# Kernel optimization log

Measured on AMD Instinct MI355X. Metric: run time of the kernel, lower is better.

Reference implementation:

```python
import jax, jax.numpy as jnp
import numpy as np

N_NODES = 50000


def gcn_layer(x, src, dst, W, b):
    # GCNConv: out = D^{-1/2} (A + I) D^{-1/2} (x W) + b
    n = x.shape[0]
    h = x @ W  # [N, C_out]
    # degree including self-loop (count of incoming edges at dst + 1)
    deg = jnp.zeros((n,), dtype=x.dtype).at[dst].add(1.0) + 1.0
    dinv_sqrt = jax.lax.rsqrt(deg)
    norm = dinv_sqrt[src] * dinv_sqrt[dst]  # [E]
    agg = jax.ops.segment_sum(h[src] * norm[:, None], dst, num_segments=n)
    # self-loop contribution: norm_ii = 1/deg_i
    agg = agg + h * (dinv_sqrt * dinv_sqrt)[:, None]
    return agg + b


def setup_inputs() -> dict:
    key = jax.random.key(0)
    k1, k2, k3, k4, k5, k6 = jax.random.split(key, 6)
    in_c, hid_c, out_c = 128, 128, 64
    x = jax.random.normal(k1, (N_NODES, in_c), dtype=jnp.float32)
    edge_index = jax.random.randint(k2, (2, 600000), 0, N_NODES, dtype=jnp.int64)
    W1 = jax.random.normal(k3, (in_c, hid_c), dtype=jnp.float32) * (1.0 / np.sqrt(in_c))
    b1 = jnp.zeros((hid_c,), dtype=jnp.float32)
    W2 = jax.random.normal(k4, (hid_c, out_c), dtype=jnp.float32) * (1.0 / np.sqrt(hid_c))
    b2 = jnp.zeros((out_c,), dtype=jnp.float32)
    return {"x": x, "edge_index": edge_index, "W1": W1, "b1": b1, "W2": W2, "b2": b2}


def reference(x, edge_index, W1, b1, W2, b2):
    src, dst = edge_index[0], edge_index[1]
    h = gcn_layer(x, src, dst, W1, b1)
    h = jax.nn.relu(h)
    out = gcn_layer(h, src, dst, W2, b2)
    return out
```

## Files before the change

kernel.cpp:

```cpp
#include <hip/hip_runtime.h>

#define IN_C 128
#define HID_C 128
#define OUT_C 64
#define CAP 40
#define LSTR 40

typedef unsigned int uint;
typedef unsigned short ushort;
typedef __attribute__((ext_vector_type(8))) short short8;
typedef __attribute__((ext_vector_type(4))) float f32x4;

__device__ __forceinline__ float bf2f(ushort u) {
    return __uint_as_float(((uint)u) << 16);
}
__device__ __forceinline__ float bfl(uint u) {
    return __uint_as_float(u << 16);
}
__device__ __forceinline__ float bfh(uint u) {
    return __uint_as_float(u & 0xffff0000u);
}
__device__ __forceinline__ ushort f2bf(float f) {
    uint u = __float_as_uint(f);
    return (ushort)((u + 0x7fffu + ((u >> 16) & 1u)) >> 16);
}


__global__ void prep0_kernel(int* __restrict__ cursor, int n,
                             const float* __restrict__ W1, ushort* __restrict__ w1h,
                             ushort* __restrict__ w1l, const float* __restrict__ W2,
                             ushort* __restrict__ w2h, ushort* __restrict__ w2l) {
    int idx = blockIdx.x * blockDim.x + threadIdx.x;
    if (idx < n) {
        cursor[idx] = 0;
    } else if (idx < n + 128 * 128) {
        int i1 = idx - n;
        int k = i1 >> 7, c = i1 & 127;
        float w = W1[i1];
        ushort h = f2bf(w);
        ushort l = f2bf(w - bf2f(h));
        w1h[c * 128 + k] = h;
        w1l[c * 128 + k] = l;
    } else if (idx < n + 128 * 128 + 128 * 64) {
        int i2 = idx - n - 128 * 128;
        int k = i2 >> 6, c = i2 & 63;
        float w = W2[i2];
        ushort h = f2bf(w);
        ushort l = f2bf(w - bf2f(h));
        w2h[c * 128 + k] = h;
        w2l[c * 128 + k] = l;
    }
}


__global__ __launch_bounds__(256) void gemm1_edge_kernel(
    const float* __restrict__ A, const ushort* __restrict__ BTh,
    const ushort* __restrict__ BTl, ushort* __restrict__ C, int M, int gblocks,
    const int* __restrict__ src, const int* __restrict__ dst,
    int* __restrict__ cursor, int* __restrict__ csr_src, int E) {
    constexpr int BN = 128;
    constexpr int NT = BN / 16;
    __shared__ ushort sAh[64 * LSTR], sAl[64 * LSTR];
    __shared__ ushort sBh[BN * LSTR], sBl[BN * LSTR];

    const int tid = threadIdx.x;

    if (blockIdx.x >= gblocks) {
        int e = (blockIdx.x - gblocks) * 256 + tid;
        if (e < E) {
            unsigned s = (unsigned)src[e];
            unsigned d = (unsigned)dst[e];
            if (s < (unsigned)M && d < (unsigned)M) {
                int p = atomicAdd(&cursor[d], 1);
                if (p < CAP) csr_src[d * CAP + p] = (int)s;
            }
        }
        return;
    }

    const int w = tid >> 6;
    const int lane = tid & 63;
    const int m = lane & 15;
    const int quad = lane >> 4;
    const int r0 = blockIdx.x * 64;

    f32x4 acc[NT];
#pragma unroll
    for (int t = 0; t < NT; ++t) acc[t] = (f32x4){0.f, 0.f, 0.f, 0.f};

    for (int k0 = 0; k0 < 128; k0 += 32) {
#pragma unroll
        for (int it = 0; it < 2; ++it) {
            int idx = tid + it * 256;
            int row = idx >> 3;
            int c4 = idx & 7;
            int grow = r0 + row;
            float4 v = make_float4(0.f, 0.f, 0.f, 0.f);
            if (grow < M) v = *(const float4*)&A[(size_t)grow * 128 + k0 + c4 * 4];
            ushort h0 = f2bf(v.x), h1 = f2bf(v.y), h2 = f2bf(v.z), h3 = f2bf(v.w);
            ushort l0 = f2bf(v.x - bf2f(h0)), l1 = f2bf(v.y - bf2f(h1));
            ushort l2 = f2bf(v.z - bf2f(h2)), l3 = f2bf(v.w - bf2f(h3));
            *(ushort4*)&sAh[row * LSTR + c4 * 4] = make_ushort4(h0, h1, h2, h3);
            *(ushort4*)&sAl[row * LSTR + c4 * 4] = make_ushort4(l0, l1, l2, l3);
        }
        for (int idx = tid; idx < BN * 4; idx += 256) {
            int row = idx >> 2;
            int c = idx & 3;
            *(uint4*)&sBh[row * LSTR + c * 8] = *(const uint4*)&BTh[row * 128 + k0 + c * 8];
            *(uint4*)&sBl[row * LSTR + c * 8] = *(const uint4*)&BTl[row * 128 + k0 + c * 8];
        }
        __syncthreads();

        short8 ah = *(const short8*)&sAh[(w * 16 + m) * LSTR + quad * 8];
        short8 al = *(const short8*)&sAl[(w * 16 + m) * LSTR + quad * 8];
#pragma unroll
        for (int t = 0; t < NT; ++t) {
            short8 bh = *(const short8*)&sBh[(t * 16 + m) * LSTR + quad * 8];
            short8 bl = *(const short8*)&sBl[(t * 16 + m) * LSTR + quad * 8];
            acc[t] = __builtin_amdgcn_mfma_f32_16x16x32_bf16(ah, bh, acc[t], 0, 0, 0);
            acc[t] = __builtin_amdgcn_mfma_f32_16x16x32_bf16(al, bh, acc[t], 0, 0, 0);
            acc[t] = __builtin_amdgcn_mfma_f32_16x16x32_bf16(ah, bl, acc[t], 0, 0, 0);
        }
        __syncthreads();
    }

#pragma unroll
    for (int t = 0; t < NT; ++t) {
#pragma unroll
        for (int r = 0; r < 4; ++r) {
            int row = r0 + w * 16 + quad * 4 + r;
            if (row < M) C[(size_t)row * BN + t * 16 + m] = f2bf(acc[t][r]);
        }
    }
}


#define ACC8(v, nn)                                     \
    {                                                   \
        a0 += (nn) * bfl((v).x); a1 += (nn) * bfh((v).x); \
        a2 += (nn) * bfl((v).y); a3 += (nn) * bfh((v).y); \
        a4 += (nn) * bfl((v).z); a5 += (nn) * bfh((v).z); \
        a6 += (nn) * bfl((v).w); a7 += (nn) * bfh((v).w); \
    }


__global__ __launch_bounds__(256) void agg_gemm2_kernel(
    const uint4* __restrict__ hx, const int* __restrict__ csr_src,
    const int* __restrict__ degs, const float* __restrict__ bias,
    const ushort* __restrict__ BTh, const ushort* __restrict__ BTl,
    ushort* __restrict__ C, int n) {
    __shared__ ushort sAf[4][64][LSTR];
    __shared__ ushort sBh[64 * LSTR], sBl[64 * LSTR];

    const int tid = threadIdx.x;
    const int w = tid >> 6;
    const int lane = tid & 63;
    const int quarter = lane >> 4;
    const int q = lane & 15;
    const int r0 = blockIdx.x * 64;

    for (int i = 0; i < 16; ++i) {
        const int lrow = w * 16 + i;
        const int node = r0 + lrow;
        uint4 u = make_uint4(0u, 0u, 0u, 0u);
        if (node < n) {
            int cnt = min(degs[node], CAP);
            float degf = (float)(cnt + 1);
            float dinv_d = rsqrtf(degf);
            int start = node * CAP;
            float a0 = 0.f, a1 = 0.f, a2 = 0.f, a3 = 0.f;
            float a4 = 0.f, a5 = 0.f, a6 = 0.f, a7 = 0.f;

            if (cnt > 0) {
                int es = (lane < cnt) ? csr_src[start + lane] : 0;
                int cs = (lane < cnt) ? degs[es] : 0;
                float en = rsqrtf((float)(cs + 1)) * dinv_d;
                int j = 0;
                for (; j + 8 <= cnt; j += 8) {
                    int sA = __shfl(es, j + quarter);
                    float nA = __shfl(en, j + quarter);
                    int sB = __shfl(es, j + 4 + quarter);
                    float nB = __shfl(en, j + 4 + quarter);
                    uint4 vA = hx[(size_t)sA * 16 + q];
                    uint4 vB = hx[(size_t)sB * 16 + q];
                    ACC8(vA, nA);
                    ACC8(vB, nB);
                }
                if (j < cnt) {
                    int k0 = j + quarter;
                    int s0 = __shfl(es, k0);
                    float n0 = __shfl(en, k0);
                    n0 = (k0 < cnt) ? n0 : 0.f;
                    uint4 v0 = hx[(size_t)s0 * 16 + q];
                    ACC8(v0, n0);
                    if (j + 4 < cnt) {
                        int k1 = j + 4 + quarter;
                        int s1 = __shfl(es, k1);
                        float n1 = __shfl(en, k1);
                        n1 = (k1 < cnt) ? n1 : 0.f;
                        uint4 v1 = hx[(size_t)s1 * 16 + q];
                        ACC8(v1, n1);
                    }
                }
            }

#pragma unroll
            for (int d = 16; d <= 32; d <<= 1) {
                a0 += __shfl_xor(a0, d); a1 += __shfl_xor(a1, d);
                a2 += __shfl_xor(a2, d); a3 += __shfl_xor(a3, d);
                a4 += __shfl_xor(a4, d); a5 += __shfl_xor(a5, d);
                a6 += __shfl_xor(a6, d); a7 += __shfl_xor(a7, d);
            }
            if (quarter == 0) {
                uint4 sv = hx[(size_t)node * 16 + q];
                float sn = 1.0f / degf;
                const float4* b4 = (const float4*)bias;
                float4 bA = b4[2 * q], bB = b4[2 * q + 1];
                float o0 = fmaxf(a0 + bfl(sv.x) * sn + bA.x, 0.f);
                float o1 = fmaxf(a1 + bfh(sv.x) * sn + bA.y, 0.f);
                float o2 = fmaxf(a2 + bfl(sv.y) * sn + bA.z, 0.f);
                float o3 = fmaxf(a3 + bfh(sv.y) * sn + bA.w, 0.f);
                float o4 = fmaxf(a4 + bfl(sv.z) * sn + bB.x, 0.f);
                float o5 = fmaxf(a5 + bfh(sv.z) * sn + bB.y, 0.f);
                float o6 = fmaxf(a6 + bfl(sv.w) * sn + bB.z, 0.f);
                float o7 = fmaxf(a7 + bfh(sv.w) * sn + bB.w, 0.f);
                u.x = (uint)f2bf(o0) | ((uint)f2bf(o1) << 16);
                u.y = (uint)f2bf(o2) | ((uint)f2bf(o3) << 16);
                u.z = (uint)f2bf(o4) | ((uint)f2bf(o5) << 16);
                u.w = (uint)f2bf(o6) | ((uint)f2bf(o7) << 16);
            }
        }
        if (quarter == 0) {
            *(uint4*)&sAf[q >> 2][lrow][(q & 3) * 8] = u;
        }
    }

    f32x4 acc[4];
#pragma unroll
    for (int t = 0; t < 4; ++t) acc[t] = (f32x4){0.f, 0.f, 0.f, 0.f};

    for (int k0 = 0; k0 < 128; k0 += 32) {
        {
            int row = tid >> 2;
            int c = tid & 3;
            *(uint4*)&sBh[row * LSTR + c * 8] = *(const uint4*)&BTh[row * 128 + k0 + c * 8];
            *(uint4*)&sBl[row * LSTR + c * 8] = *(const uint4*)&BTl[row * 128 + k0 + c * 8];
        }
        __syncthreads();

        short8 ah = *(const short8*)&sAf[k0 >> 5][w * 16 + q][quarter * 8];
#pragma unroll
        for (int t = 0; t < 4; ++t) {
            short8 bh = *(const short8*)&sBh[(t * 16 + q) * LSTR + quarter * 8];
            short8 bl = *(const short8*)&sBl[(t * 16 + q) * LSTR + quarter * 8];
            acc[t] = __builtin_amdgcn_mfma_f32_16x16x32_bf16(ah, bh, acc[t], 0, 0, 0);
            acc[t] = __builtin_amdgcn_mfma_f32_16x16x32_bf16(ah, bl, acc[t], 0, 0, 0);
        }
        __syncthreads();
    }

#pragma unroll
    for (int t = 0; t < 4; ++t) {
#pragma unroll
        for (int r = 0; r < 4; ++r) {
            int row = r0 + w * 16 + quarter * 4 + r;
            if (row < n) C[(size_t)row * 64 + t * 16 + q] = f2bf(acc[t][r]);
        }
    }
}


__global__ __launch_bounds__(256) void agg64_kernel(
    const uint4* __restrict__ hx, const int* __restrict__ csr_src,
    const int* __restrict__ degs, const float* __restrict__ bias,
    float* __restrict__ out, int n) {
    int node = blockIdx.x * 4 + (threadIdx.x >> 6);
    if (node >= n) return;
    int lane = threadIdx.x & 63;
    int oct = lane >> 3;
    int q = lane & 7;
    int cnt = min(degs[node], CAP);
    float degf = (float)(cnt + 1);
    float dinv_d = rsqrtf(degf);
    int start = node * CAP;
    float a0 = 0.f, a1 = 0.f, a2 = 0.f, a3 = 0.f;
    float a4 = 0.f, a5 = 0.f, a6 = 0.f, a7 = 0.f;

    if (cnt > 0) {
        int es = (lane < cnt) ? csr_src[start + lane] : 0;
        int cs = (lane < cnt) ? degs[es] : 0;
        float en = rsqrtf((float)(cs + 1)) * dinv_d;
        int j = 0;
        for (; j + 16 <= cnt; j += 16) {
            int sA = __shfl(es, j + oct);
            float nA = __shfl(en, j + oct);
            int sB = __shfl(es, j + 8 + oct);
            float nB = __shfl(en, j + 8 + oct);
            uint4 vA = hx[(size_t)sA * 8 + q];
            uint4 vB = hx[(size_t)sB * 8 + q];
            ACC8(vA, nA);
            ACC8(vB, nB);
        }
        if (j < cnt) {
            int k0 = j + oct;
            int s0 = __shfl(es, k0);
            float n0 = __shfl(en, k0);
            n0 = (k0 < cnt) ? n0 : 0.f;
            uint4 v0 = hx[(size_t)s0 * 8 + q];
            ACC8(v0, n0);
            if (j + 8 < cnt) {
                int k1 = j + 8 + oct;
                int s1 = __shfl(es, k1);
                float n1 = __shfl(en, k1);
                n1 = (k1 < cnt) ? n1 : 0.f;
                uint4 v1 = hx[(size_t)s1 * 8 + q];
                ACC8(v1, n1);
            }
        }
    }

#pragma unroll
    for (int d = 8; d <= 32; d <<= 1) {
        a0 += __shfl_xor(a0, d); a1 += __shfl_xor(a1, d);
        a2 += __shfl_xor(a2, d); a3 += __shfl_xor(a3, d);
        a4 += __shfl_xor(a4, d); a5 += __shfl_xor(a5, d);
        a6 += __shfl_xor(a6, d); a7 += __shfl_xor(a7, d);
    }
    if (oct == 0) {
        uint4 sv = hx[(size_t)node * 8 + q];
        float sn = 1.0f / degf;
        const float4* b4 = (const float4*)bias;
        float4 bA = b4[2 * q], bB = b4[2 * q + 1];
        float4 oA, oB;
        oA.x = a0 + bfl(sv.x) * sn + bA.x;
        oA.y = a1 + bfh(sv.x) * sn + bA.y;
        oA.z = a2 + bfl(sv.y) * sn + bA.z;
        oA.w = a3 + bfh(sv.y) * sn + bA.w;
        oB.x = a4 + bfl(sv.z) * sn + bB.x;
        oB.y = a5 + bfh(sv.z) * sn + bB.y;
        oB.z = a6 + bfl(sv.w) * sn + bB.z;
        oB.w = a7 + bfh(sv.w) * sn + bB.w;
        float4* o4 = (float4*)out;
        o4[(size_t)node * 16 + 2 * q] = oA;
        o4[(size_t)node * 16 + 2 * q + 1] = oB;
    }
}


extern "C" void kernel_launch(void* const* d_in, const int* in_sizes, int n_in,
                              void* d_out, int out_size, void* d_ws, size_t ws_size,
                              hipStream_t stream) {
    (void)n_in; (void)out_size; (void)ws_size;
    const float* x  = (const float*)d_in[0];
    const int*   ei = (const int*)d_in[1];
    const float* W1 = (const float*)d_in[2];
    const float* b1 = (const float*)d_in[3];
    const float* W2 = (const float*)d_in[4];
    const float* b2 = (const float*)d_in[5];
    float* out = (float*)d_out;

    const int n = in_sizes[0] / IN_C;
    const int E = in_sizes[1] / 2;
    const int* src = ei;
    const int* dst = ei + E;

    char* ws = (char*)d_ws;
    size_t off = 0;
    auto alloc = [&](size_t bytes) -> void* {
        void* p = ws + off;
        off += (bytes + 1023) & ~(size_t)1023;
        return p;
    };

    ushort* w1h     = (ushort*)alloc(128 * 128 * 2);
    ushort* w1l     = (ushort*)alloc(128 * 128 * 2);
    ushort* w2h     = (ushort*)alloc(64 * 128 * 2);
    ushort* w2l     = (ushort*)alloc(64 * 128 * 2);
    int*    cursor  = (int*)   alloc((size_t)n * 4);
    int*    csr_src = (int*)   alloc((size_t)n * CAP * 4);
    ushort* h1      = (ushort*)alloc((size_t)n * HID_C * 2);
    ushort* h2      = (ushort*)alloc((size_t)n * HID_C * 2);

    const int gblocks = (n + 63) / 64;
    const int EB = (E + 255) / 256;
    const int ablocks = (n + 3) / 4;

    prep0_kernel<<<(n + 128 * 128 + 128 * 64 + 255) / 256, 256, 0, stream>>>(
        cursor, n, W1, w1h, w1l, W2, w2h, w2l);
    gemm1_edge_kernel<<<gblocks + EB, 256, 0, stream>>>(x, w1h, w1l, h1, n, gblocks,
                                                        src, dst, cursor, csr_src, E);
    agg_gemm2_kernel<<<gblocks, 256, 0, stream>>>((const uint4*)h1, csr_src, cursor,
                                                  b1, w2h, w2l, h2, n);
    agg64_kernel<<<ablocks, 256, 0, stream>>>((const uint4*)h2, csr_src, cursor,
                                              b2, out, n);
}
```

Before: 187.8 us.

## Process four nodes per wave in fused aggregation-GEMM2 and halve block rows

The layer-1 aggregation inside the fused agg+GEMM2 kernel now gives each 16-lane quarter-wave its own node instead of spreading one node's edges across the whole wave. That removes the cross-quarter shuffle reduction and lets all four quarters write rows directly. Each block now covers 32 rows instead of 64, doubling the grid, and the MFMA tile split becomes 2x2 across warps. Edge lists and degrees for the next node group are prefetched while the current group runs. A risk is load imbalance and wasted loads, because each quarter loops to the maximum degree among the four nodes sharing a wave.

```diff
diff --git a/kernel.cpp b/kernel.cpp
--- a/kernel.cpp
+++ b/kernel.cpp
@@ -149,95 +149,116 @@
     const int* __restrict__ degs, const float* __restrict__ bias,
     const ushort* __restrict__ BTh, const ushort* __restrict__ BTl,
     ushort* __restrict__ C, int n) {
-    __shared__ ushort sAf[4][64][LSTR];
+    __shared__ ushort sAf[4][32][LSTR];
     __shared__ ushort sBh[64 * LSTR], sBl[64 * LSTR];
 
     const int tid = threadIdx.x;
     const int w = tid >> 6;
     const int lane = tid & 63;
-    const int quarter = lane >> 4;
-    const int q = lane & 15;
-    const int r0 = blockIdx.x * 64;
-
-    for (int i = 0; i < 16; ++i) {
-        const int lrow = w * 16 + i;
+    const int q4 = lane >> 4;
+    const int c16 = lane & 15;
+    const int r0 = blockIdx.x * 32;
+
+    int nd = 0, t0 = 0, t1 = 0, t2 = 0;
+    {
+        int node = r0 + w * 8 + q4;
+        bool valid = node < n;
+        nd = valid ? degs[node] : 0;
+        size_t base = (size_t)node * CAP;
+        t0 = valid ? csr_src[base + c16] : 0;
+        t1 = valid ? csr_src[base + 16 + c16] : 0;
+        t2 = (valid && c16 < 8) ? csr_src[base + 32 + c16] : 0;
+    }
+
+    for (int g = 0; g < 2; ++g) {
+        const int lrow = w * 8 + g * 4 + q4;
         const int node = r0 + lrow;
-        uint4 u = make_uint4(0u, 0u, 0u, 0u);
-        if (node < n) {
-            int cnt = min(degs[node], CAP);
-            float degf = (float)(cnt + 1);
-            float dinv_d = rsqrtf(degf);
-            int start = node * CAP;
-            float a0 = 0.f, a1 = 0.f, a2 = 0.f, a3 = 0.f;
-            float a4 = 0.f, a5 = 0.f, a6 = 0.f, a7 = 0.f;
-
-            if (cnt > 0) {
-                int es = (lane < cnt) ? csr_src[start + lane] : 0;
-                int cs = (lane < cnt) ? degs[es] : 0;
-                float en = rsqrtf((float)(cs + 1)) * dinv_d;
-                int j = 0;
-                for (; j + 8 <= cnt; j += 8) {
-                    int sA = __shfl(es, j + quarter);
-                    float nA = __shfl(en, j + quarter);
-                    int sB = __shfl(es, j + 4 + quarter);
-                    float nB = __shfl(en, j + 4 + quarter);
-                    uint4 vA = hx[(size_t)sA * 16 + q];
-                    uint4 vB = hx[(size_t)sB * 16 + q];
-                    ACC8(vA, nA);
-                    ACC8(vB, nB);
-                }
-                if (j < cnt) {
-                    int k0 = j + quarter;
-                    int s0 = __shfl(es, k0);
-                    float n0 = __shfl(en, k0);
-                    n0 = (k0 < cnt) ? n0 : 0.f;
-                    uint4 v0 = hx[(size_t)s0 * 16 + q];
-                    ACC8(v0, n0);
-                    if (j + 4 < cnt) {
-                        int k1 = j + 4 + quarter;
-                        int s1 = __shfl(es, k1);
-                        float n1 = __shfl(en, k1);
-                        n1 = (k1 < cnt) ? n1 : 0.f;
-                        uint4 v1 = hx[(size_t)s1 * 16 + q];
-                        ACC8(v1, n1);
-                    }
-                }
+        const bool valid = node < n;
+        const int cnt = min(nd, CAP);
+        const float degf = (float)(cnt + 1);
+        const float dinv = rsqrtf(degf);
+        int es0 = (c16 < cnt) ? t0 : 0;
+        int es1 = (16 + c16 < cnt) ? t1 : 0;
+        int es2 = (32 + c16 < cnt) ? t2 : 0;
+        int d0 = degs[es0];
+        int d1 = degs[es1];
+        int d2 = degs[es2];
+        uint4 sv = make_uint4(0u, 0u, 0u, 0u);
+        if (valid) sv = hx[(size_t)node * 16 + c16];
+        int nd_n = 0, t0n = 0, t1n = 0, t2n = 0;
+        if (g + 1 < 2) {
+            int node_n = r0 + w * 8 + (g + 1) * 4 + q4;
+            bool vn = node_n < n;
+            nd_n = vn ? degs[node_n] : 0;
+            size_t base_n = (size_t)node_n * CAP;
+            t0n = vn ? csr_src[base_n + c16] : 0;
+            t1n = vn ? csr_src[base_n + 16 + c16] : 0;
+            t2n = (vn && c16 < 8) ? csr_src[base_n + 32 + c16] : 0;
+        }
+        float en0 = (c16 < cnt) ? rsqrtf((float)(d0 + 1)) * dinv : 0.f;
+        float en1 = (16 + c16 < cnt) ? rsqrtf((float)(d1 + 1)) * dinv : 0.f;
+        float en2 = (32 + c16 < cnt) ? rsqrtf((float)(d2 + 1)) * dinv : 0.f;
+        int cm = cnt;
+        cm = max(cm, __shfl_xor(cm, 16));
+        cm = max(cm, __shfl_xor(cm, 32));
+
+        float a0 = 0.f, a1 = 0.f, a2 = 0.f, a3 = 0.f;
+        float a4 = 0.f, a5 = 0.f, a6 = 0.f, a7 = 0.f;
+
+        auto EDGE = [&](int kk, int& s, float& wt) {
+            if (kk < 16) {
+                s = __shfl(es0, (q4 << 4) + kk);
+                wt = __shfl(en0, (q4 << 4) + kk);
+            } else if (kk < 32) {
+                s = __shfl(es1, (q4 << 4) + kk - 16);
+                wt = __shfl(en1, (q4 << 4) + kk - 16);
+            } else {
+                s = __shfl(es2, (q4 << 4) + kk - 32);
+                wt = __shfl(en2, (q4 << 4) + kk - 32);
             }
-
-#pragma unroll
-            for (int d = 16; d <= 32; d <<= 1) {
-                a0 += __shfl_xor(a0, d); a1 += __shfl_xor(a1, d);
-                a2 += __shfl_xor(a2, d); a3 += __shfl_xor(a3, d);
-                a4 += __shfl_xor(a4, d); a5 += __shfl_xor(a5, d);
-                a6 += __shfl_xor(a6, d); a7 += __shfl_xor(a7, d);
-            }
-            if (quarter == 0) {
-                uint4 sv = hx[(size_t)node * 16 + q];
-                float sn = 1.0f / degf;
-                const float4* b4 = (const float4*)bias;
-                float4 bA = b4[2 * q], bB = b4[2 * q + 1];
-                float o0 = fmaxf(a0 + bfl(sv.x) * sn + bA.x, 0.f);
-                float o1 = fmaxf(a1 + bfh(sv.x) * sn + bA.y, 0.f);
-                float o2 = fmaxf(a2 + bfl(sv.y) * sn + bA.z, 0.f);
-                float o3 = fmaxf(a3 + bfh(sv.y) * sn + bA.w, 0.f);
-                float o4 = fmaxf(a4 + bfl(sv.z) * sn + bB.x, 0.f);
-                float o5 = fmaxf(a5 + bfh(sv.z) * sn + bB.y, 0.f);
-                float o6 = fmaxf(a6 + bfl(sv.w) * sn + bB.z, 0.f);
-                float o7 = fmaxf(a7 + bfh(sv.w) * sn + bB.w, 0.f);
-                u.x = (uint)f2bf(o0) | ((uint)f2bf(o1) << 16);
-                u.y = (uint)f2bf(o2) | ((uint)f2bf(o3) << 16);
-                u.z = (uint)f2bf(o4) | ((uint)f2bf(o5) << 16);
-                u.w = (uint)f2bf(o6) | ((uint)f2bf(o7) << 16);
-            }
-        }
-        if (quarter == 0) {
-            *(uint4*)&sAf[q >> 2][lrow][(q & 3) * 8] = u;
-        }
-    }
-
-    f32x4 acc[4];
-#pragma unroll
-    for (int t = 0; t < 4; ++t) acc[t] = (f32x4){0.f, 0.f, 0.f, 0.f};
+        };
+
+        int k = 0;
+        for (; k + 2 <= cm; k += 2) {
+            int sA; float nA; EDGE(k, sA, nA);
+            int sB; float nB; EDGE(k + 1, sB, nB);
+            uint4 vA = hx[(size_t)sA * 16 + c16];
+            uint4 vB = hx[(size_t)sB * 16 + c16];
+            ACC8(vA, nA);
+            ACC8(vB, nB);
+        }
+        if (k < cm) {
+            int sA; float nA; EDGE(k, sA, nA);
+            uint4 vA = hx[(size_t)sA * 16 + c16];
+            ACC8(vA, nA);
+        }
+
+        float sn = 1.0f / degf;
+        const float4* b4 = (const float4*)bias;
+        float4 bA = b4[2 * c16], bB = b4[2 * c16 + 1];
+        float o0 = fmaxf(a0 + bfl(sv.x) * sn + bA.x, 0.f);
+        float o1 = fmaxf(a1 + bfh(sv.x) * sn + bA.y, 0.f);
+        float o2 = fmaxf(a2 + bfl(sv.y) * sn + bA.z, 0.f);
+        float o3 = fmaxf(a3 + bfh(sv.y) * sn + bA.w, 0.f);
+        float o4 = fmaxf(a4 + bfl(sv.z) * sn + bB.x, 0.f);
+        float o5 = fmaxf(a5 + bfh(sv.z) * sn + bB.y, 0.f);
+        float o6 = fmaxf(a6 + bfl(sv.w) * sn + bB.z, 0.f);
+        float o7 = fmaxf(a7 + bfh(sv.w) * sn + bB.w, 0.f);
+        uint4 u;
+        u.x = (uint)f2bf(o0) | ((uint)f2bf(o1) << 16);
+        u.y = (uint)f2bf(o2) | ((uint)f2bf(o3) << 16);
+        u.z = (uint)f2bf(o4) | ((uint)f2bf(o5) << 16);
+        u.w = (uint)f2bf(o6) | ((uint)f2bf(o7) << 16);
+        *(uint4*)&sAf[c16 >> 2][lrow][(c16 & 3) * 8] = u;
+
+        nd = nd_n; t0 = t0n; t1 = t1n; t2 = t2n;
+    }
+
+    const int wm = w >> 1;
+    const int wn = w & 1;
+    f32x4 acc[2];
+#pragma unroll
+    for (int t = 0; t < 2; ++t) acc[t] = (f32x4){0.f, 0.f, 0.f, 0.f};
 
     for (int k0 = 0; k0 < 128; k0 += 32) {
         {
@@ -248,11 +269,12 @@
         }
         __syncthreads();
 
-        short8 ah = *(const short8*)&sAf[k0 >> 5][w * 16 + q][quarter * 8];
-#pragma unroll
-        for (int t = 0; t < 4; ++t) {
-            short8 bh = *(const short8*)&sBh[(t * 16 + q) * LSTR + quarter * 8];
-            short8 bl = *(const short8*)&sBl[(t * 16 + q) * LSTR + quarter * 8];
+        short8 ah = *(const short8*)&sAf[k0 >> 5][wm * 16 + c16][q4 * 8];
+#pragma unroll
+        for (int t = 0; t < 2; ++t) {
+            int tt = wn * 2 + t;
+            short8 bh = *(const short8*)&sBh[(tt * 16 + c16) * LSTR + q4 * 8];
+            short8 bl = *(const short8*)&sBl[(tt * 16 + c16) * LSTR + q4 * 8];
             acc[t] = __builtin_amdgcn_mfma_f32_16x16x32_bf16(ah, bh, acc[t], 0, 0, 0);
             acc[t] = __builtin_amdgcn_mfma_f32_16x16x32_bf16(ah, bl, acc[t], 0, 0, 0);
         }
@@ -260,11 +282,11 @@
     }
 
 #pragma unroll
-    for (int t = 0; t < 4; ++t) {
+    for (int t = 0; t < 2; ++t) {
 #pragma unroll
         for (int r = 0; r < 4; ++r) {
-            int row = r0 + w * 16 + quarter * 4 + r;
-            if (row < n) C[(size_t)row * 64 + t * 16 + q] = f2bf(acc[t][r]);
+            int row = r0 + wm * 16 + q4 * 4 + r;
+            if (row < n) C[(size_t)row * 64 + (wn * 2 + t) * 16 + c16] = f2bf(acc[t][r]);
         }
     }
 }
@@ -383,13 +405,14 @@
 
     const int gblocks = (n + 63) / 64;
     const int EB = (E + 255) / 256;
+    const int fblocks = (n + 31) / 32;
     const int ablocks = (n + 3) / 4;
 
     prep0_kernel<<<(n + 128 * 128 + 128 * 64 + 255) / 256, 256, 0, stream>>>(
         cursor, n, W1, w1h, w1l, W2, w2h, w2l);
     gemm1_edge_kernel<<<gblocks + EB, 256, 0, stream>>>(x, w1h, w1l, h1, n, gblocks,
                                                         src, dst, cursor, csr_src, E);
-    agg_gemm2_kernel<<<gblocks, 256, 0, stream>>>((const uint4*)h1, csr_src, cursor,
+    agg_gemm2_kernel<<<fblocks, 256, 0, stream>>>((const uint4*)h1, csr_src, cursor,
                                                   b1, w2h, w2l, h2, n);
     agg64_kernel<<<ablocks, 256, 0, stream>>>((const uint4*)h2, csr_src, cursor,
                                               b2, out, n);
```

New measurement: 168.7 us. -10.2%, faster.
